# Optimization experiments

Hardware: AMD Instinct MI355X
Metric: run time of the kernel (lower is better)

The kernel has to match this reference:

```python
import jax, jax.numpy as jnp
import numpy as np

N, E, D = 100000, 1000000, 128  # nodes, edges, feature dim (in=hidden=out)
BN_EPS = 1e-5


def setup_inputs() -> dict:
    key = jax.random.key(0)
    ks = jax.random.split(key, 6)
    inp = {
        "x": jax.random.normal(ks[0], (N, D), dtype=jnp.float32),
        "edge_src": jax.random.randint(ks[1], (E,), 0, N),
        "edge_dst": jax.random.randint(ks[2], (E,), 0, N),
    }
    # GraphConv weights (xavier-ish) and biases for 3 layers
    for i in range(3):
        inp[f"W{i}"] = jax.random.normal(ks[3 + i], (D, D), dtype=jnp.float32) * np.float32(1.0 / np.sqrt(D))
        inp[f"b{i}"] = jnp.zeros((D,), dtype=jnp.float32)
    # BatchNorm (eval mode) params/buffers for the 2 inter-layer BNs
    for i in range(2):
        inp[f"bn_gamma{i}"] = jnp.ones((D,), dtype=jnp.float32)
        inp[f"bn_beta{i}"] = jnp.zeros((D,), dtype=jnp.float32)
        inp[f"bn_mean{i}"] = jnp.zeros((D,), dtype=jnp.float32)
        inp[f"bn_var{i}"] = jnp.ones((D,), dtype=jnp.float32)
    return inp


def _gcn_forward(x, edge_src, edge_dst, Ws, bs, bns):
    n = x.shape[0]
    ones = jnp.ones((edge_src.shape[0],), x.dtype)
    # DGL GraphConv norm='both': D_out^{-1/2} on source, D_in^{-1/2} on dest, degrees clamped to >=1
    deg_out = jnp.clip(jax.ops.segment_sum(ones, edge_src, num_segments=n), 1.0)
    deg_in = jnp.clip(jax.ops.segment_sum(ones, edge_dst, num_segments=n), 1.0)
    norm_src = deg_out ** -0.5
    norm_dst = deg_in ** -0.5
    h = x
    L = len(Ws)
    for i in range(L):
        hs = (h * norm_src[:, None]) @ Ws[i]                     # [N, D] dense transform first
        agg = jax.ops.segment_sum(hs[edge_src], edge_dst, num_segments=n)  # SpMM: gather + scatter-add
        h = agg * norm_dst[:, None] + bs[i]
        if i < L - 1:  # BN (eval) + activation between layers; dropout=0 -> no-op
            g, bta, m, v = bns[i]
            h = (h - m) * jax.lax.rsqrt(v + BN_EPS) * g + bta
            h = jax.nn.relu(h)
    return h


def reference(x, edge_src, edge_dst, W0, b0, W1, b1, W2, b2,
              bn_gamma0, bn_beta0, bn_mean0, bn_var0,
              bn_gamma1, bn_beta1, bn_mean1, bn_var1):
    Ws = (W0, W1, W2)
    bs = (b0, b1, b2)
    bns = ((bn_gamma0, bn_beta0, bn_mean0, bn_var0),
           (bn_gamma1, bn_beta1, bn_mean1, bn_var1))
    return _gcn_forward(x, edge_src, edge_dst, Ws, bs, bns)
```

## Files before the change

kernel.cpp:

```cpp
#include <hip/hip_runtime.h>
#include <hip/hip_fp16.h>
#include <math.h>

#define D 128
#define NSL 32
#define PBU 25088

typedef _Float16 half8 __attribute__((ext_vector_type(8)));
typedef float f32x4 __attribute__((ext_vector_type(4)));

__device__ inline uint pack_f16x2(float a, float b) {
  __half2 h = __floats2half2_rn(a, b);
  return *reinterpret_cast<uint*>(&h);
}
__device__ inline float2 unpack_f16x2(uint p) {
  __half2 h = *reinterpret_cast<__half2*>(&p);
  return __half22float2(h);
}
__device__ inline uint mdiv40(uint x, uint M) {
  return (uint)(((unsigned long long)x * M) >> 40);
}


__global__ __launch_bounds__(1024) void k_build1(const int* __restrict__ esrc,
                                                 const int* __restrict__ edst,
                                                 const float* __restrict__ W0,
                                                 const float* __restrict__ W1,
                                                 const float* __restrict__ W2,
                                                 const float* __restrict__ b0,
                                                 const float* __restrict__ b1,
                                                 const float* __restrict__ b2,
                                                 const float* __restrict__ g0,
                                                 const float* __restrict__ be0,
                                                 const float* __restrict__ mu0,
                                                 const float* __restrict__ vr0,
                                                 const float* __restrict__ g1,
                                                 const float* __restrict__ be1,
                                                 const float* __restrict__ mu1,
                                                 const float* __restrict__ vr1,
                                                 uint* __restrict__ pd,
                                                 uint* __restrict__ ps,
                                                 uchar* __restrict__ rank8,
                                                 ushort* __restrict__ Wt,
                                                 float* __restrict__ CA,
                                                 float* __restrict__ CB,
                                                 int E, int SB) {
  __shared__ uint h[PBU];
  const int b = blockIdx.x;
  const int t = threadIdx.x;
  if (b < 32) {
    for (int j = t; j < PBU; j += 1024) h[j] = 0u;
    __syncthreads();
    const int i0 = b * SB, i1 = min(i0 + SB, E);
    for (int i = i0 + t; i < i1; i += 1024) {
      const int d = edst[i];
      const uint sh = (uint)(d & 3) * 8u;
      const uint old = atomicAdd(&h[d >> 2], 1u << sh);
      rank8[i] = (uchar)((old >> sh) & 0xffu);
    }
    __syncthreads();
    uint* p = pd + (size_t)b * PBU;
    for (int j = t; j < PBU; j += 1024) p[j] = h[j];
  } else if (b < 64) {
    const int sl = b - 32;
    for (int j = t; j < PBU; j += 1024) h[j] = 0u;
    __syncthreads();
    const int i0 = sl * SB, i1 = min(i0 + SB, E);
    for (int i = i0 + t; i < i1; i += 1024) {
      const int s = esrc[i];
      atomicAdd(&h[s >> 2], 1u << ((uint)(s & 3) * 8u));
    }
    __syncthreads();
    uint* p = ps + (size_t)sl * PBU;
    for (int j = t; j < PBU; j += 1024) p[j] = h[j];
  } else if (b < 112) {
    const int li = (b - 64) * 1024 + t;
    const int l = li >> 14;
    const int i = li & 16383;
    const int n = i >> 7, k = i & 127;
    const float* W = (l == 0) ? W0 : ((l == 1) ? W1 : W2);
    Wt[li] = __half_as_ushort(__float2half_rn(W[k * D + n]));
  } else if (t < D) {
    const int c = t;
    float A0 = g0[c] * rsqrtf(vr0[c] + 1e-5f);
    CA[c] = A0;
    CB[c] = (b0[c] - mu0[c]) * A0 + be0[c];
    float A1 = g1[c] * rsqrtf(vr1[c] + 1e-5f);
    CA[D + c] = A1;
    CB[D + c] = (b1[c] - mu1[c]) * A1 + be1[c];
    CA[2 * D + c] = 1.f;
    CB[2 * D + c] = b2[c];
  }
}


__global__ __launch_bounds__(256) void k_build2(uint* __restrict__ pd,
                                                const uint* __restrict__ ps,
                                                int* __restrict__ totd,
                                                float* __restrict__ ns,
                                                float* __restrict__ nd,
                                                int* __restrict__ csum, int N) {
  __shared__ int sd[256];
  const int t = threadIdx.x;
  const int j = blockIdx.x * 256 + t;
  const int n0 = j * 4;
  uint r0 = 0, r1 = 0, r2 = 0, r3 = 0;
  uint s0 = 0, s1 = 0, s2 = 0, s3 = 0;
#pragma unroll
  for (int sl = 0; sl < NSL; ++sl) {
    const uint v = pd[(size_t)sl * PBU + j];
    pd[(size_t)sl * PBU + j] = r0 | (r1 << 8) | (r2 << 16) | (r3 << 24);
    r0 += v & 0xffu; r1 += (v >> 8) & 0xffu; r2 += (v >> 16) & 0xffu; r3 += (v >> 24) & 0xffu;
    const uint w = ps[(size_t)sl * PBU + j];
    s0 += w & 0xffu; s1 += (w >> 8) & 0xffu; s2 += (w >> 16) & 0xffu; s3 += (w >> 24) & 0xffu;
  }
  const uint rr[4] = {r0, r1, r2, r3};
  const uint ss[4] = {s0, s1, s2, s3};
  int tot = 0;
#pragma unroll
  for (int k = 0; k < 4; ++k) {
    if (n0 + k < N) {
      totd[n0 + k] = (int)rr[k];
      nd[n0 + k] = rsqrtf((float)max(rr[k], 1u));
      ns[n0 + k] = rsqrtf((float)max(ss[k], 1u));
      tot += (int)rr[k];
    }
  }
  sd[t] = tot; __syncthreads();
  for (int off = 128; off > 0; off >>= 1) {
    if (t < off) sd[t] += sd[t + off];
    __syncthreads();
  }
  if (t == 0) csum[blockIdx.x] = sd[0];
}


__global__ void k_scan_serial(int* __restrict__ csum, int nch,
                              int* __restrict__ rofs, int n) {
  if (blockIdx.x == 0 && threadIdx.x == 0) {
    int run = 0;
    for (int b = 0; b < nch; ++b) { int v = csum[b]; csum[b] = run; run += v; }
    rofs[n] = run;
  }
}

__global__ __launch_bounds__(256) void k_scan_final(const int* __restrict__ totd,
                                                    const int* __restrict__ csum,
                                                    int* __restrict__ rofs, int n) {
  __shared__ int sd[256];
  const int b = blockIdx.x, t = threadIdx.x;
  const int base = b * 1024 + t * 4;
  int v[4]; int s = 0;
#pragma unroll
  for (int i = 0; i < 4; ++i) { v[i] = (base + i < n) ? totd[base + i] : 0; s += v[i]; }
  sd[t] = s; __syncthreads();
  for (int off = 1; off < 256; off <<= 1) {
    int x = (t >= off) ? sd[t - off] : 0;
    __syncthreads();
    sd[t] += x;
    __syncthreads();
  }
  int o = sd[t] - s + csum[b];
#pragma unroll
  for (int i = 0; i < 4; ++i) {
    if (base + i < n) { rofs[base + i] = o; o += v[i]; }
  }
}


__global__ void k_scatter2(const int* __restrict__ esrc, const int* __restrict__ edst,
                           const uchar* __restrict__ rank8,
                           const uint* __restrict__ pd,
                           const int* __restrict__ rofs, int* __restrict__ csr,
                           int E, uint Msb) {
  const int i = blockIdx.x * 256 + threadIdx.x;
  if (i >= E) return;
  const int d = edst[i];
  const uint sl = mdiv40((uint)i, Msb);
  const uint pk = pd[(size_t)sl * PBU + (d >> 2)];
  const uint pfx = (pk >> ((uint)(d & 3) * 8u)) & 0xffu;
  csr[rofs[d] + (int)pfx + (int)rank8[i]] = esrc[i];
}


__global__ __launch_bounds__(256) void k_gemm32(const float* __restrict__ X,
                                                const ushort* __restrict__ Wt,
                                                const float* __restrict__ ns,
                                                ushort* __restrict__ out, int M) {
  const int lane = threadIdx.x & 63;
  const int wv = threadIdx.x >> 6;
  const int m0 = (blockIdx.x * 4 + wv) * 32;
  if (m0 >= M) return;
  const int lr = lane & 15;
  const int kg = (lane >> 4) * 8;

  half8 hf[2][4];
  const half8 hz = {};
#pragma unroll
  for (int mt = 0; mt < 2; ++mt) {
    const int row = m0 + mt * 16 + lr;
    if (row < M) {
      const float s = ns[row];
#pragma unroll
      for (int kt = 0; kt < 4; ++kt) {
        const float4 a = *reinterpret_cast<const float4*>(X + (size_t)row * D + kt * 32 + kg);
        const float4 b = *reinterpret_cast<const float4*>(X + (size_t)row * D + kt * 32 + kg + 4);
        half8 hv;
        hv[0] = (_Float16)(a.x * s); hv[1] = (_Float16)(a.y * s);
        hv[2] = (_Float16)(a.z * s); hv[3] = (_Float16)(a.w * s);
        hv[4] = (_Float16)(b.x * s); hv[5] = (_Float16)(b.y * s);
        hv[6] = (_Float16)(b.z * s); hv[7] = (_Float16)(b.w * s);
        hf[mt][kt] = hv;
      }
    } else {
#pragma unroll
      for (int kt = 0; kt < 4; ++kt) hf[mt][kt] = hz;
    }
  }

  f32x4 acc[8][2];
#pragma unroll
  for (int nt = 0; nt < 8; ++nt) { acc[nt][0] = (f32x4)(0.f); acc[nt][1] = (f32x4)(0.f); }

#pragma unroll
  for (int nt = 0; nt < 8; ++nt) {
    const ushort* wb = Wt + (size_t)(nt * 16 + lr) * D + kg;
#pragma unroll
    for (int kt = 0; kt < 4; ++kt) {
      half8 wf = *reinterpret_cast<const half8*>(wb + kt * 32);
      acc[nt][0] = __builtin_amdgcn_mfma_f32_16x16x32_f16(wf, hf[0][kt], acc[nt][0], 0, 0, 0);
      acc[nt][1] = __builtin_amdgcn_mfma_f32_16x16x32_f16(wf, hf[1][kt], acc[nt][1], 0, 0, 0);
    }
  }

  const int mo = lane & 15;
  const int no = (lane >> 4) * 4;
#pragma unroll
  for (int mt = 0; mt < 2; ++mt) {
    const int row = m0 + mt * 16 + mo;
    if (row < M) {
#pragma unroll
      for (int nt = 0; nt < 8; ++nt) {
        uint2 u;
        u.x = pack_f16x2(acc[nt][mt][0], acc[nt][mt][1]);
        u.y = pack_f16x2(acc[nt][mt][2], acc[nt][mt][3]);
        *reinterpret_cast<uint2*>(out + (size_t)row * D + nt * 16 + no) = u;
      }
    }
  }
}


__global__ __launch_bounds__(256) void k_gemm16(const ushort* __restrict__ A,
                                                const ushort* __restrict__ Wt,
                                                ushort* __restrict__ out, int M) {
  const int lane = threadIdx.x & 63;
  const int wv = threadIdx.x >> 6;
  const int m0 = (blockIdx.x * 4 + wv) * 32;
  if (m0 >= M) return;
  const int lr = lane & 15;
  const int kg = (lane >> 4) * 8;

  half8 hf[2][4];
  const half8 hz = {};
#pragma unroll
  for (int mt = 0; mt < 2; ++mt) {
    const int row = m0 + mt * 16 + lr;
    const bool ok = row < M;
#pragma unroll
    for (int kt = 0; kt < 4; ++kt)
      hf[mt][kt] = ok ? *reinterpret_cast<const half8*>(A + (size_t)row * D + kt * 32 + kg)
                      : hz;
  }

  f32x4 acc[8][2];
#pragma unroll
  for (int nt = 0; nt < 8; ++nt) { acc[nt][0] = (f32x4)(0.f); acc[nt][1] = (f32x4)(0.f); }

#pragma unroll
  for (int nt = 0; nt < 8; ++nt) {
    const ushort* wb = Wt + (size_t)(nt * 16 + lr) * D + kg;
#pragma unroll
    for (int kt = 0; kt < 4; ++kt) {
      half8 wf = *reinterpret_cast<const half8*>(wb + kt * 32);
      acc[nt][0] = __builtin_amdgcn_mfma_f32_16x16x32_f16(wf, hf[0][kt], acc[nt][0], 0, 0, 0);
      acc[nt][1] = __builtin_amdgcn_mfma_f32_16x16x32_f16(wf, hf[1][kt], acc[nt][1], 0, 0, 0);
    }
  }

  const int mo = lane & 15;
  const int no = (lane >> 4) * 4;
#pragma unroll
  for (int mt = 0; mt < 2; ++mt) {
    const int row = m0 + mt * 16 + mo;
    if (row < M) {
#pragma unroll
      for (int nt = 0; nt < 8; ++nt) {
        uint2 u;
        u.x = pack_f16x2(acc[nt][mt][0], acc[nt][mt][1]);
        u.y = pack_f16x2(acc[nt][mt][2], acc[nt][mt][3]);
        *reinterpret_cast<uint2*>(out + (size_t)row * D + nt * 16 + no) = u;
      }
    }
  }
}


__global__ __launch_bounds__(256) void k_spmm16(const uint* __restrict__ hs,
                                                const int* __restrict__ csr,
                                                const int* __restrict__ rofs,
                                                const float* __restrict__ nd,
                                                const float* __restrict__ ns,
                                                const float* __restrict__ CA,
                                                const float* __restrict__ CB,
                                                float* __restrict__ outf,
                                                uint* __restrict__ hnext,
                                                int N, int last) {
  const int t = threadIdx.x;
  const int lane = t & 63;
  const int c16 = lane & 15;
  const int gb = lane & ~15;
  const int d = blockIdx.x * 16 + (t >> 4);
  if (d >= N) return;
  const int beg = rofs[d], end = rofs[d + 1];

  float acc[8];
#pragma unroll
  for (int j = 0; j < 8; ++j) acc[j] = 0.f;

  for (int base = beg; base < end; base += 16) {
    const int len = min(16, end - base);
    const int idx = csr[min(base + c16, end - 1)];
#pragma unroll 1
    for (int j = 0; j < len; j += 4) {
      const int l1 = min(j + 1, len - 1), l2 = min(j + 2, len - 1), l3 = min(j + 3, len - 1);
      const int s0 = __shfl(idx, gb + j);
      const int s1 = __shfl(idx, gb + l1);
      const int s2 = __shfl(idx, gb + l2);
      const int s3 = __shfl(idx, gb + l3);
      const float w1 = (j + 1 < len) ? 1.f : 0.f;
      const float w2 = (j + 2 < len) ? 1.f : 0.f;
      const float w3 = (j + 3 < len) ? 1.f : 0.f;
      const uint4 v0 = *reinterpret_cast<const uint4*>(hs + (size_t)s0 * 64 + c16 * 4);
      const uint4 v1 = *reinterpret_cast<const uint4*>(hs + (size_t)s1 * 64 + c16 * 4);
      const uint4 v2 = *reinterpret_cast<const uint4*>(hs + (size_t)s2 * 64 + c16 * 4);
      const uint4 v3 = *reinterpret_cast<const uint4*>(hs + (size_t)s3 * 64 + c16 * 4);
#pragma unroll
      for (int q = 0; q < 4; ++q) {
        const uint u0 = (&v0.x)[q], u1 = (&v1.x)[q], u2 = (&v2.x)[q], u3 = (&v3.x)[q];
        const float2 a0 = unpack_f16x2(u0);
        const float2 a1 = unpack_f16x2(u1);
        const float2 a2 = unpack_f16x2(u2);
        const float2 a3 = unpack_f16x2(u3);
        acc[q * 2]     += a0.x;
        acc[q * 2 + 1] += a0.y;
        acc[q * 2]     = fmaf(a1.x, w1, acc[q * 2]);
        acc[q * 2 + 1] = fmaf(a1.y, w1, acc[q * 2 + 1]);
        acc[q * 2]     = fmaf(a2.x, w2, acc[q * 2]);
        acc[q * 2 + 1] = fmaf(a2.y, w2, acc[q * 2 + 1]);
        acc[q * 2]     = fmaf(a3.x, w3, acc[q * 2]);
        acc[q * 2 + 1] = fmaf(a3.y, w3, acc[q * 2 + 1]);
      }
    }
  }

  const float ndv = nd[d];
  const float4 ca0 = *reinterpret_cast<const float4*>(CA + c16 * 8);
  const float4 ca1 = *reinterpret_cast<const float4*>(CA + c16 * 8 + 4);
  const float4 cb0 = *reinterpret_cast<const float4*>(CB + c16 * 8);
  const float4 cb1 = *reinterpret_cast<const float4*>(CB + c16 * 8 + 4);
  float r[8];
  r[0] = acc[0] * ndv * ca0.x + cb0.x;
  r[1] = acc[1] * ndv * ca0.y + cb0.y;
  r[2] = acc[2] * ndv * ca0.z + cb0.z;
  r[3] = acc[3] * ndv * ca0.w + cb0.w;
  r[4] = acc[4] * ndv * ca1.x + cb1.x;
  r[5] = acc[5] * ndv * ca1.y + cb1.y;
  r[6] = acc[6] * ndv * ca1.z + cb1.z;
  r[7] = acc[7] * ndv * ca1.w + cb1.w;
  if (!last) {
    const float s = ns[d];
#pragma unroll
    for (int j = 0; j < 8; ++j) r[j] = fmaxf(r[j], 0.f) * s;
    uint4 u;
    u.x = pack_f16x2(r[0], r[1]);
    u.y = pack_f16x2(r[2], r[3]);
    u.z = pack_f16x2(r[4], r[5]);
    u.w = pack_f16x2(r[6], r[7]);
    *reinterpret_cast<uint4*>(hnext + (size_t)d * 64 + c16 * 4) = u;
  } else {
    float4 o0 = make_float4(r[0], r[1], r[2], r[3]);
    float4 o1 = make_float4(r[4], r[5], r[6], r[7]);
    *reinterpret_cast<float4*>(outf + (size_t)d * D + c16 * 8) = o0;
    *reinterpret_cast<float4*>(outf + (size_t)d * D + c16 * 8 + 4) = o1;
  }
}


extern "C" void kernel_launch(void* const* d_in, const int* in_sizes, int n_in,
                              void* d_out, int out_size, void* d_ws, size_t ws_size,
                              hipStream_t stream) {
  const float* x = (const float*)d_in[0];
  const int* esrc = (const int*)d_in[1];
  const int* edst = (const int*)d_in[2];
  const float* W0 = (const float*)d_in[3];
  const float* b0 = (const float*)d_in[4];
  const float* W1 = (const float*)d_in[5];
  const float* b1 = (const float*)d_in[6];
  const float* W2 = (const float*)d_in[7];
  const float* b2 = (const float*)d_in[8];
  const float* g0 = (const float*)d_in[9];
  const float* be0 = (const float*)d_in[10];
  const float* m0 = (const float*)d_in[11];
  const float* v0 = (const float*)d_in[12];
  const float* g1 = (const float*)d_in[13];
  const float* be1 = (const float*)d_in[14];
  const float* m1 = (const float*)d_in[15];
  const float* v1 = (const float*)d_in[16];
  const int N = in_sizes[0] / D;
  const int E = in_sizes[1];

  const int SB = (E + NSL - 1) / NSL;
  const uint Msb = (uint)(((1ULL << 40) + (unsigned long long)SB - 1) / (unsigned long long)SB);

  char* p = (char*)d_ws;
  auto carve = [&](size_t bytes) {
    char* r = p;
    p += (bytes + 255) & ~(size_t)255;
    return (void*)r;
  };
  uint* hs16 = (uint*)carve((size_t)N * 64 * 4);
  ushort* Wt = (ushort*)carve((size_t)3 * D * D * 2);
  float* CA = (float*)carve((size_t)3 * D * 4);
  float* CB = (float*)carve((size_t)3 * D * 4);
  float* ns = (float*)carve((size_t)N * 4);
  float* nd = (float*)carve((size_t)N * 4);
  uint* pd = (uint*)carve((size_t)NSL * PBU * 4);
  uint* ps = (uint*)carve((size_t)NSL * PBU * 4);
  uchar* rank8 = (uchar*)carve((size_t)E);
  int* totd = (int*)carve((size_t)N * 4);
  int* rofs = (int*)carve((size_t)(N + 1) * 4);
  const int nch = (N + 1023) / 1024;
  int* csum = (int*)carve((size_t)nch * 4);
  int* csr = (int*)carve((size_t)E * 4);
  uint* bufA = (uint*)d_out;

  k_build1<<<113, 1024, 0, stream>>>(esrc, edst, W0, W1, W2, b0, b1, b2,
                                     g0, be0, m0, v0, g1, be1, m1, v1,
                                     pd, ps, rank8, Wt, CA, CB, E, SB);
  k_build2<<<nch, 256, 0, stream>>>(pd, ps, totd, ns, nd, csum, N);
  k_scan_serial<<<1, 1, 0, stream>>>(csum, nch, rofs, N);
  k_scan_final<<<nch, 256, 0, stream>>>(totd, csum, rofs, N);
  k_scatter2<<<(E + 255) / 256, 256, 0, stream>>>(esrc, edst, rank8, pd, rofs, csr, E, Msb);

  const int gb = (N + 127) / 128;
  const int sb = (N + 15) / 16;
  k_gemm32<<<gb, 256, 0, stream>>>(x, Wt, ns, (ushort*)hs16, N);
  k_spmm16<<<sb, 256, 0, stream>>>(hs16, csr, rofs, nd, ns, CA, CB, nullptr, bufA, N, 0);
  k_gemm16<<<gb, 256, 0, stream>>>((const ushort*)bufA, Wt + 16384, (ushort*)hs16, N);
  k_spmm16<<<sb, 256, 0, stream>>>(hs16, csr, rofs, nd, ns, CA + D, CB + D, nullptr, bufA, N, 0);
  k_gemm16<<<gb, 256, 0, stream>>>((const ushort*)bufA, Wt + 32768, (ushort*)hs16, N);
  k_spmm16<<<sb, 256, 0, stream>>>(hs16, csr, rofs, nd, ns, CA + 2 * D, CB + 2 * D,
                                   (float*)d_out, nullptr, N, 1);
}
```

Baseline: 267.6 us.

## Fuse all graph-build, GEMM and SpMM stages into one cooperative persistent kernel

Replaces the eleven separate launches (histograms, prefix scans, CSR scatter, three GEMMs, three SpMMs) with a single cooperative kernel of 256 blocks of 1024 threads, separated by grid.sync barriers. The degree histogram is split into 128 slices per direction instead of 32 so every block takes part. Block-level scans become wave-level shuffle scans. The CSR scatter runs alongside the first GEMM. The goal is to remove launch gaps and inter-kernel drain/fill. The cost is several grid-wide barriers, and a fixed grid with one large block per CU that may reduce occupancy and latency hiding in the gather-heavy SpMM phases.

```diff
diff --git a/kernel.cpp b/kernel.cpp
--- a/kernel.cpp
+++ b/kernel.cpp
@@ -1,10 +1,15 @@
 #include <hip/hip_runtime.h>
 #include <hip/hip_fp16.h>
+#include <hip/hip_cooperative_groups.h>
 #include <math.h>
 
 #define D 128
-#define NSL 32
+#define NSL 128
 #define PBU 25088
+#define GRID 256
+#define BLK 1024
+
+namespace cg = cooperative_groups;
 
 typedef _Float16 half8 __attribute__((ext_vector_type(8)));
 typedef float f32x4 __attribute__((ext_vector_type(4)));
@@ -21,179 +26,67 @@
   return (uint)(((unsigned long long)x * M) >> 40);
 }
 
-
-__global__ __launch_bounds__(1024) void k_build1(const int* __restrict__ esrc,
-                                                 const int* __restrict__ edst,
-                                                 const float* __restrict__ W0,
-                                                 const float* __restrict__ W1,
-                                                 const float* __restrict__ W2,
-                                                 const float* __restrict__ b0,
-                                                 const float* __restrict__ b1,
-                                                 const float* __restrict__ b2,
-                                                 const float* __restrict__ g0,
-                                                 const float* __restrict__ be0,
-                                                 const float* __restrict__ mu0,
-                                                 const float* __restrict__ vr0,
-                                                 const float* __restrict__ g1,
-                                                 const float* __restrict__ be1,
-                                                 const float* __restrict__ mu1,
-                                                 const float* __restrict__ vr1,
-                                                 uint* __restrict__ pd,
-                                                 uint* __restrict__ ps,
-                                                 uchar* __restrict__ rank8,
-                                                 ushort* __restrict__ Wt,
-                                                 float* __restrict__ CA,
-                                                 float* __restrict__ CB,
-                                                 int E, int SB) {
-  __shared__ uint h[PBU];
-  const int b = blockIdx.x;
-  const int t = threadIdx.x;
-  if (b < 32) {
-    for (int j = t; j < PBU; j += 1024) h[j] = 0u;
-    __syncthreads();
-    const int i0 = b * SB, i1 = min(i0 + SB, E);
-    for (int i = i0 + t; i < i1; i += 1024) {
-      const int d = edst[i];
-      const uint sh = (uint)(d & 3) * 8u;
-      const uint old = atomicAdd(&h[d >> 2], 1u << sh);
-      rank8[i] = (uchar)((old >> sh) & 0xffu);
-    }
-    __syncthreads();
-    uint* p = pd + (size_t)b * PBU;
-    for (int j = t; j < PBU; j += 1024) p[j] = h[j];
-  } else if (b < 64) {
-    const int sl = b - 32;
-    for (int j = t; j < PBU; j += 1024) h[j] = 0u;
-    __syncthreads();
-    const int i0 = sl * SB, i1 = min(i0 + SB, E);
-    for (int i = i0 + t; i < i1; i += 1024) {
-      const int s = esrc[i];
-      atomicAdd(&h[s >> 2], 1u << ((uint)(s & 3) * 8u));
-    }
-    __syncthreads();
-    uint* p = ps + (size_t)sl * PBU;
-    for (int j = t; j < PBU; j += 1024) p[j] = h[j];
-  } else if (b < 112) {
-    const int li = (b - 64) * 1024 + t;
-    const int l = li >> 14;
-    const int i = li & 16383;
-    const int n = i >> 7, k = i & 127;
-    const float* W = (l == 0) ? W0 : ((l == 1) ? W1 : W2);
-    Wt[li] = __half_as_ushort(__float2half_rn(W[k * D + n]));
-  } else if (t < D) {
-    const int c = t;
-    float A0 = g0[c] * rsqrtf(vr0[c] + 1e-5f);
-    CA[c] = A0;
-    CB[c] = (b0[c] - mu0[c]) * A0 + be0[c];
-    float A1 = g1[c] * rsqrtf(vr1[c] + 1e-5f);
-    CA[D + c] = A1;
-    CB[D + c] = (b1[c] - mu1[c]) * A1 + be1[c];
-    CA[2 * D + c] = 1.f;
-    CB[2 * D + c] = b2[c];
-  }
-}
-
-
-__global__ __launch_bounds__(256) void k_build2(uint* __restrict__ pd,
-                                                const uint* __restrict__ ps,
-                                                int* __restrict__ totd,
-                                                float* __restrict__ ns,
-                                                float* __restrict__ nd,
-                                                int* __restrict__ csum, int N) {
-  __shared__ int sd[256];
-  const int t = threadIdx.x;
-  const int j = blockIdx.x * 256 + t;
-  const int n0 = j * 4;
-  uint r0 = 0, r1 = 0, r2 = 0, r3 = 0;
-  uint s0 = 0, s1 = 0, s2 = 0, s3 = 0;
-#pragma unroll
-  for (int sl = 0; sl < NSL; ++sl) {
-    const uint v = pd[(size_t)sl * PBU + j];
-    pd[(size_t)sl * PBU + j] = r0 | (r1 << 8) | (r2 << 16) | (r3 << 24);
-    r0 += v & 0xffu; r1 += (v >> 8) & 0xffu; r2 += (v >> 16) & 0xffu; r3 += (v >> 24) & 0xffu;
-    const uint w = ps[(size_t)sl * PBU + j];
-    s0 += w & 0xffu; s1 += (w >> 8) & 0xffu; s2 += (w >> 16) & 0xffu; s3 += (w >> 24) & 0xffu;
-  }
-  const uint rr[4] = {r0, r1, r2, r3};
-  const uint ss[4] = {s0, s1, s2, s3};
-  int tot = 0;
-#pragma unroll
-  for (int k = 0; k < 4; ++k) {
-    if (n0 + k < N) {
-      totd[n0 + k] = (int)rr[k];
-      nd[n0 + k] = rsqrtf((float)max(rr[k], 1u));
-      ns[n0 + k] = rsqrtf((float)max(ss[k], 1u));
-      tot += (int)rr[k];
-    }
-  }
-  sd[t] = tot; __syncthreads();
-  for (int off = 128; off > 0; off >>= 1) {
-    if (t < off) sd[t] += sd[t + off];
-    __syncthreads();
-  }
-  if (t == 0) csum[blockIdx.x] = sd[0];
-}
-
-
-__global__ void k_scan_serial(int* __restrict__ csum, int nch,
-                              int* __restrict__ rofs, int n) {
-  if (blockIdx.x == 0 && threadIdx.x == 0) {
-    int run = 0;
-    for (int b = 0; b < nch; ++b) { int v = csum[b]; csum[b] = run; run += v; }
-    rofs[n] = run;
-  }
-}
-
-__global__ __launch_bounds__(256) void k_scan_final(const int* __restrict__ totd,
-                                                    const int* __restrict__ csum,
-                                                    int* __restrict__ rofs, int n) {
-  __shared__ int sd[256];
-  const int b = blockIdx.x, t = threadIdx.x;
-  const int base = b * 1024 + t * 4;
-  int v[4]; int s = 0;
-#pragma unroll
-  for (int i = 0; i < 4; ++i) { v[i] = (base + i < n) ? totd[base + i] : 0; s += v[i]; }
-  sd[t] = s; __syncthreads();
-  for (int off = 1; off < 256; off <<= 1) {
-    int x = (t >= off) ? sd[t - off] : 0;
-    __syncthreads();
-    sd[t] += x;
-    __syncthreads();
-  }
-  int o = sd[t] - s + csum[b];
-#pragma unroll
-  for (int i = 0; i < 4; ++i) {
-    if (base + i < n) { rofs[base + i] = o; o += v[i]; }
-  }
-}
-
-
-__global__ void k_scatter2(const int* __restrict__ esrc, const int* __restrict__ edst,
-                           const uchar* __restrict__ rank8,
-                           const uint* __restrict__ pd,
-                           const int* __restrict__ rofs, int* __restrict__ csr,
-                           int E, uint Msb) {
-  const int i = blockIdx.x * 256 + threadIdx.x;
-  if (i >= E) return;
-  const int d = edst[i];
-  const uint sl = mdiv40((uint)i, Msb);
-  const uint pk = pd[(size_t)sl * PBU + (d >> 2)];
-  const uint pfx = (pk >> ((uint)(d & 3) * 8u)) & 0xffu;
-  csr[rofs[d] + (int)pfx + (int)rank8[i]] = esrc[i];
-}
-
-
-__global__ __launch_bounds__(256) void k_gemm32(const float* __restrict__ X,
-                                                const ushort* __restrict__ Wt,
-                                                const float* __restrict__ ns,
-                                                ushort* __restrict__ out, int M) {
-  const int lane = threadIdx.x & 63;
-  const int wv = threadIdx.x >> 6;
-  const int m0 = (blockIdx.x * 4 + wv) * 32;
+struct MegaArgs {
+  const float* x; const int* esrc; const int* edst;
+  const float* W0; const float* b0; const float* W1; const float* b1;
+  const float* W2; const float* b2;
+  const float* g0; const float* be0; const float* mu0; const float* vr0;
+  const float* g1; const float* be1; const float* mu1; const float* vr1;
+  uint* pd; uint* ps; uchar* rank8;
+  ushort* Wt; float* CA; float* CB;
+  float* ns; float* nd; int* totd; int* csum; int* rofs;
+  int* csr; uint* hs16; uint* bufA; float* outF;
+  int N, E, SB, nch2; uint Msb;
+};
+
+__device__ inline void gemm_wave_f16(const ushort* __restrict__ A,
+                                     const ushort* __restrict__ Wt,
+                                     ushort* __restrict__ out, int M, int w, int lane) {
+  const int m0 = w * 32;
   if (m0 >= M) return;
   const int lr = lane & 15;
   const int kg = (lane >> 4) * 8;
-
+  half8 hf[2][4];
+  const half8 hz = {};
+#pragma unroll
+  for (int mt = 0; mt < 2; ++mt) {
+    const int row = m0 + mt * 16 + lr;
+    const bool ok = row < M;
+#pragma unroll
+    for (int kt = 0; kt < 4; ++kt)
+      hf[mt][kt] = ok ? *reinterpret_cast<const half8*>(A + (size_t)row * D + kt * 32 + kg) : hz;
+  }
+  const int no = (lane >> 4) * 4;
+#pragma unroll
+  for (int nt = 0; nt < 8; ++nt) {
+    f32x4 a0 = (f32x4)(0.f), a1 = (f32x4)(0.f);
+    const ushort* wb = Wt + (size_t)(nt * 16 + lr) * D + kg;
+#pragma unroll
+    for (int kt = 0; kt < 4; ++kt) {
+      half8 wf = *reinterpret_cast<const half8*>(wb + kt * 32);
+      a0 = __builtin_amdgcn_mfma_f32_16x16x32_f16(wf, hf[0][kt], a0, 0, 0, 0);
+      a1 = __builtin_amdgcn_mfma_f32_16x16x32_f16(wf, hf[1][kt], a1, 0, 0, 0);
+    }
+    const int r0 = m0 + lr, r1 = m0 + 16 + lr;
+    if (r0 < M) {
+      uint2 u; u.x = pack_f16x2(a0[0], a0[1]); u.y = pack_f16x2(a0[2], a0[3]);
+      *reinterpret_cast<uint2*>(out + (size_t)r0 * D + nt * 16 + no) = u;
+    }
+    if (r1 < M) {
+      uint2 u; u.x = pack_f16x2(a1[0], a1[1]); u.y = pack_f16x2(a1[2], a1[3]);
+      *reinterpret_cast<uint2*>(out + (size_t)r1 * D + nt * 16 + no) = u;
+    }
+  }
+}
+
+__device__ inline void gemm_wave_f32(const float* __restrict__ X,
+                                     const ushort* __restrict__ Wt,
+                                     const float* __restrict__ ns,
+                                     ushort* __restrict__ out, int M, int w, int lane) {
+  const int m0 = w * 32;
+  if (m0 >= M) return;
+  const int lr = lane & 15;
+  const int kg = (lane >> 4) * 8;
   half8 hf[2][4];
   const half8 hz = {};
 #pragma unroll
@@ -217,209 +110,268 @@
       for (int kt = 0; kt < 4; ++kt) hf[mt][kt] = hz;
     }
   }
-
-  f32x4 acc[8][2];
-#pragma unroll
-  for (int nt = 0; nt < 8; ++nt) { acc[nt][0] = (f32x4)(0.f); acc[nt][1] = (f32x4)(0.f); }
-
+  const int no = (lane >> 4) * 4;
 #pragma unroll
   for (int nt = 0; nt < 8; ++nt) {
+    f32x4 a0 = (f32x4)(0.f), a1 = (f32x4)(0.f);
     const ushort* wb = Wt + (size_t)(nt * 16 + lr) * D + kg;
 #pragma unroll
     for (int kt = 0; kt < 4; ++kt) {
       half8 wf = *reinterpret_cast<const half8*>(wb + kt * 32);
-      acc[nt][0] = __builtin_amdgcn_mfma_f32_16x16x32_f16(wf, hf[0][kt], acc[nt][0], 0, 0, 0);
-      acc[nt][1] = __builtin_amdgcn_mfma_f32_16x16x32_f16(wf, hf[1][kt], acc[nt][1], 0, 0, 0);
-    }
-  }
-
-  const int mo = lane & 15;
-  const int no = (lane >> 4) * 4;
-#pragma unroll
-  for (int mt = 0; mt < 2; ++mt) {
-    const int row = m0 + mt * 16 + mo;
-    if (row < M) {
-#pragma unroll
-      for (int nt = 0; nt < 8; ++nt) {
-        uint2 u;
-        u.x = pack_f16x2(acc[nt][mt][0], acc[nt][mt][1]);
-        u.y = pack_f16x2(acc[nt][mt][2], acc[nt][mt][3]);
-        *reinterpret_cast<uint2*>(out + (size_t)row * D + nt * 16 + no) = u;
-      }
-    }
-  }
-}
-
-
-__global__ __launch_bounds__(256) void k_gemm16(const ushort* __restrict__ A,
-                                                const ushort* __restrict__ Wt,
-                                                ushort* __restrict__ out, int M) {
-  const int lane = threadIdx.x & 63;
-  const int wv = threadIdx.x >> 6;
-  const int m0 = (blockIdx.x * 4 + wv) * 32;
-  if (m0 >= M) return;
-  const int lr = lane & 15;
-  const int kg = (lane >> 4) * 8;
-
-  half8 hf[2][4];
-  const half8 hz = {};
-#pragma unroll
-  for (int mt = 0; mt < 2; ++mt) {
-    const int row = m0 + mt * 16 + lr;
-    const bool ok = row < M;
-#pragma unroll
-    for (int kt = 0; kt < 4; ++kt)
-      hf[mt][kt] = ok ? *reinterpret_cast<const half8*>(A + (size_t)row * D + kt * 32 + kg)
-                      : hz;
-  }
-
-  f32x4 acc[8][2];
-#pragma unroll
-  for (int nt = 0; nt < 8; ++nt) { acc[nt][0] = (f32x4)(0.f); acc[nt][1] = (f32x4)(0.f); }
-
-#pragma unroll
-  for (int nt = 0; nt < 8; ++nt) {
-    const ushort* wb = Wt + (size_t)(nt * 16 + lr) * D + kg;
-#pragma unroll
-    for (int kt = 0; kt < 4; ++kt) {
-      half8 wf = *reinterpret_cast<const half8*>(wb + kt * 32);
-      acc[nt][0] = __builtin_amdgcn_mfma_f32_16x16x32_f16(wf, hf[0][kt], acc[nt][0], 0, 0, 0);
-      acc[nt][1] = __builtin_amdgcn_mfma_f32_16x16x32_f16(wf, hf[1][kt], acc[nt][1], 0, 0, 0);
-    }
-  }
-
-  const int mo = lane & 15;
-  const int no = (lane >> 4) * 4;
-#pragma unroll
-  for (int mt = 0; mt < 2; ++mt) {
-    const int row = m0 + mt * 16 + mo;
-    if (row < M) {
-#pragma unroll
-      for (int nt = 0; nt < 8; ++nt) {
-        uint2 u;
-        u.x = pack_f16x2(acc[nt][mt][0], acc[nt][mt][1]);
-        u.y = pack_f16x2(acc[nt][mt][2], acc[nt][mt][3]);
-        *reinterpret_cast<uint2*>(out + (size_t)row * D + nt * 16 + no) = u;
-      }
-    }
-  }
-}
-
-
-__global__ __launch_bounds__(256) void k_spmm16(const uint* __restrict__ hs,
-                                                const int* __restrict__ csr,
-                                                const int* __restrict__ rofs,
-                                                const float* __restrict__ nd,
-                                                const float* __restrict__ ns,
-                                                const float* __restrict__ CA,
-                                                const float* __restrict__ CB,
-                                                float* __restrict__ outf,
-                                                uint* __restrict__ hnext,
-                                                int N, int last) {
-  const int t = threadIdx.x;
-  const int lane = t & 63;
+      a0 = __builtin_amdgcn_mfma_f32_16x16x32_f16(wf, hf[0][kt], a0, 0, 0, 0);
+      a1 = __builtin_amdgcn_mfma_f32_16x16x32_f16(wf, hf[1][kt], a1, 0, 0, 0);
+    }
+    const int r0 = m0 + lr, r1 = m0 + 16 + lr;
+    if (r0 < M) {
+      uint2 u; u.x = pack_f16x2(a0[0], a0[1]); u.y = pack_f16x2(a0[2], a0[3]);
+      *reinterpret_cast<uint2*>(out + (size_t)r0 * D + nt * 16 + no) = u;
+    }
+    if (r1 < M) {
+      uint2 u; u.x = pack_f16x2(a1[0], a1[1]); u.y = pack_f16x2(a1[2], a1[3]);
+      *reinterpret_cast<uint2*>(out + (size_t)r1 * D + nt * 16 + no) = u;
+    }
+  }
+}
+
+__device__ inline void spmm_phase(const uint* __restrict__ hs,
+                                  const int* __restrict__ csr,
+                                  const int* __restrict__ rofs,
+                                  const float* __restrict__ nd,
+                                  const float* __restrict__ ns,
+                                  const float* __restrict__ CA,
+                                  const float* __restrict__ CB,
+                                  float* __restrict__ outf,
+                                  uint* __restrict__ hnext,
+                                  int N, int gid, int lane, int last) {
   const int c16 = lane & 15;
   const int gb = lane & ~15;
-  const int d = blockIdx.x * 16 + (t >> 4);
-  if (d >= N) return;
-  const int beg = rofs[d], end = rofs[d + 1];
-
-  float acc[8];
-#pragma unroll
-  for (int j = 0; j < 8; ++j) acc[j] = 0.f;
-
-  for (int base = beg; base < end; base += 16) {
-    const int len = min(16, end - base);
-    const int idx = csr[min(base + c16, end - 1)];
+  for (int d = gid >> 4; d < N; d += (GRID * BLK) >> 4) {
+    const int beg = rofs[d], end = rofs[d + 1];
+    float acc[8];
+#pragma unroll
+    for (int j = 0; j < 8; ++j) acc[j] = 0.f;
+    for (int base = beg; base < end; base += 16) {
+      const int len = min(16, end - base);
+      const int idx = csr[min(base + c16, end - 1)];
 #pragma unroll 1
-    for (int j = 0; j < len; j += 4) {
-      const int l1 = min(j + 1, len - 1), l2 = min(j + 2, len - 1), l3 = min(j + 3, len - 1);
-      const int s0 = __shfl(idx, gb + j);
-      const int s1 = __shfl(idx, gb + l1);
-      const int s2 = __shfl(idx, gb + l2);
-      const int s3 = __shfl(idx, gb + l3);
-      const float w1 = (j + 1 < len) ? 1.f : 0.f;
-      const float w2 = (j + 2 < len) ? 1.f : 0.f;
-      const float w3 = (j + 3 < len) ? 1.f : 0.f;
-      const uint4 v0 = *reinterpret_cast<const uint4*>(hs + (size_t)s0 * 64 + c16 * 4);
-      const uint4 v1 = *reinterpret_cast<const uint4*>(hs + (size_t)s1 * 64 + c16 * 4);
-      const uint4 v2 = *reinterpret_cast<const uint4*>(hs + (size_t)s2 * 64 + c16 * 4);
-      const uint4 v3 = *reinterpret_cast<const uint4*>(hs + (size_t)s3 * 64 + c16 * 4);
-#pragma unroll
-      for (int q = 0; q < 4; ++q) {
-        const uint u0 = (&v0.x)[q], u1 = (&v1.x)[q], u2 = (&v2.x)[q], u3 = (&v3.x)[q];
-        const float2 a0 = unpack_f16x2(u0);
-        const float2 a1 = unpack_f16x2(u1);
-        const float2 a2 = unpack_f16x2(u2);
-        const float2 a3 = unpack_f16x2(u3);
-        acc[q * 2]     += a0.x;
-        acc[q * 2 + 1] += a0.y;
-        acc[q * 2]     = fmaf(a1.x, w1, acc[q * 2]);
-        acc[q * 2 + 1] = fmaf(a1.y, w1, acc[q * 2 + 1]);
-        acc[q * 2]     = fmaf(a2.x, w2, acc[q * 2]);
-        acc[q * 2 + 1] = fmaf(a2.y, w2, acc[q * 2 + 1]);
-        acc[q * 2]     = fmaf(a3.x, w3, acc[q * 2]);
-        acc[q * 2 + 1] = fmaf(a3.y, w3, acc[q * 2 + 1]);
-      }
-    }
-  }
-
-  const float ndv = nd[d];
-  const float4 ca0 = *reinterpret_cast<const float4*>(CA + c16 * 8);
-  const float4 ca1 = *reinterpret_cast<const float4*>(CA + c16 * 8 + 4);
-  const float4 cb0 = *reinterpret_cast<const float4*>(CB + c16 * 8);
-  const float4 cb1 = *reinterpret_cast<const float4*>(CB + c16 * 8 + 4);
-  float r[8];
-  r[0] = acc[0] * ndv * ca0.x + cb0.x;
-  r[1] = acc[1] * ndv * ca0.y + cb0.y;
-  r[2] = acc[2] * ndv * ca0.z + cb0.z;
-  r[3] = acc[3] * ndv * ca0.w + cb0.w;
-  r[4] = acc[4] * ndv * ca1.x + cb1.x;
-  r[5] = acc[5] * ndv * ca1.y + cb1.y;
-  r[6] = acc[6] * ndv * ca1.z + cb1.z;
-  r[7] = acc[7] * ndv * ca1.w + cb1.w;
-  if (!last) {
-    const float s = ns[d];
-#pragma unroll
-    for (int j = 0; j < 8; ++j) r[j] = fmaxf(r[j], 0.f) * s;
-    uint4 u;
-    u.x = pack_f16x2(r[0], r[1]);
-    u.y = pack_f16x2(r[2], r[3]);
-    u.z = pack_f16x2(r[4], r[5]);
-    u.w = pack_f16x2(r[6], r[7]);
-    *reinterpret_cast<uint4*>(hnext + (size_t)d * 64 + c16 * 4) = u;
-  } else {
-    float4 o0 = make_float4(r[0], r[1], r[2], r[3]);
-    float4 o1 = make_float4(r[4], r[5], r[6], r[7]);
-    *reinterpret_cast<float4*>(outf + (size_t)d * D + c16 * 8) = o0;
-    *reinterpret_cast<float4*>(outf + (size_t)d * D + c16 * 8 + 4) = o1;
-  }
+      for (int j = 0; j < len; j += 4) {
+        const int l1 = min(j + 1, len - 1), l2 = min(j + 2, len - 1), l3 = min(j + 3, len - 1);
+        const int s0 = __shfl(idx, gb + j);
+        const int s1 = __shfl(idx, gb + l1);
+        const int s2 = __shfl(idx, gb + l2);
+        const int s3 = __shfl(idx, gb + l3);
+        const float w1 = (j + 1 < len) ? 1.f : 0.f;
+        const float w2 = (j + 2 < len) ? 1.f : 0.f;
+        const float w3 = (j + 3 < len) ? 1.f : 0.f;
+        const uint4 v0 = *reinterpret_cast<const uint4*>(hs + (size_t)s0 * 64 + c16 * 4);
+        const uint4 v1 = *reinterpret_cast<const uint4*>(hs + (size_t)s1 * 64 + c16 * 4);
+        const uint4 v2 = *reinterpret_cast<const uint4*>(hs + (size_t)s2 * 64 + c16 * 4);
+        const uint4 v3 = *reinterpret_cast<const uint4*>(hs + (size_t)s3 * 64 + c16 * 4);
+#pragma unroll
+        for (int q = 0; q < 4; ++q) {
+          const float2 a0 = unpack_f16x2((&v0.x)[q]);
+          const float2 a1 = unpack_f16x2((&v1.x)[q]);
+          const float2 a2 = unpack_f16x2((&v2.x)[q]);
+          const float2 a3 = unpack_f16x2((&v3.x)[q]);
+          acc[q * 2]     += a0.x;
+          acc[q * 2 + 1] += a0.y;
+          acc[q * 2]     = fmaf(a1.x, w1, acc[q * 2]);
+          acc[q * 2 + 1] = fmaf(a1.y, w1, acc[q * 2 + 1]);
+          acc[q * 2]     = fmaf(a2.x, w2, acc[q * 2]);
+          acc[q * 2 + 1] = fmaf(a2.y, w2, acc[q * 2 + 1]);
+          acc[q * 2]     = fmaf(a3.x, w3, acc[q * 2]);
+          acc[q * 2 + 1] = fmaf(a3.y, w3, acc[q * 2 + 1]);
+        }
+      }
+    }
+    const float ndv = nd[d];
+    const float4 ca0 = *reinterpret_cast<const float4*>(CA + c16 * 8);
+    const float4 ca1 = *reinterpret_cast<const float4*>(CA + c16 * 8 + 4);
+    const float4 cb0 = *reinterpret_cast<const float4*>(CB + c16 * 8);
+    const float4 cb1 = *reinterpret_cast<const float4*>(CB + c16 * 8 + 4);
+    float r[8];
+    r[0] = acc[0] * ndv * ca0.x + cb0.x;
+    r[1] = acc[1] * ndv * ca0.y + cb0.y;
+    r[2] = acc[2] * ndv * ca0.z + cb0.z;
+    r[3] = acc[3] * ndv * ca0.w + cb0.w;
+    r[4] = acc[4] * ndv * ca1.x + cb1.x;
+    r[5] = acc[5] * ndv * ca1.y + cb1.y;
+    r[6] = acc[6] * ndv * ca1.z + cb1.z;
+    r[7] = acc[7] * ndv * ca1.w + cb1.w;
+    if (!last) {
+      const float s = ns[d];
+#pragma unroll
+      for (int j = 0; j < 8; ++j) r[j] = fmaxf(r[j], 0.f) * s;
+      uint4 u;
+      u.x = pack_f16x2(r[0], r[1]);
+      u.y = pack_f16x2(r[2], r[3]);
+      u.z = pack_f16x2(r[4], r[5]);
+      u.w = pack_f16x2(r[6], r[7]);
+      *reinterpret_cast<uint4*>(hnext + (size_t)d * 64 + c16 * 4) = u;
+    } else {
+      float4 o0 = make_float4(r[0], r[1], r[2], r[3]);
+      float4 o1 = make_float4(r[4], r[5], r[6], r[7]);
+      *reinterpret_cast<float4*>(outf + (size_t)d * D + c16 * 8) = o0;
+      *reinterpret_cast<float4*>(outf + (size_t)d * D + c16 * 8 + 4) = o1;
+    }
+  }
+}
+
+
+__global__ __launch_bounds__(BLK) void k_mega(MegaArgs a) {
+  __shared__ uint h[PBU];
+  cg::grid_group grid = cg::this_grid();
+  const int t = threadIdx.x;
+  const int bid = blockIdx.x;
+  const int gid = bid * BLK + t;
+  const int lane = t & 63;
+  const int wid = gid >> 6;
+
+  for (int j = t; j < PBU; j += BLK) h[j] = 0u;
+  __syncthreads();
+  {
+    const int sl = (bid < NSL) ? bid : bid - NSL;
+    const int i0 = sl * a.SB, i1 = min(i0 + a.SB, a.E);
+    if (bid < NSL) {
+      for (int i = i0 + t; i < i1; i += BLK) {
+        const int d = a.edst[i];
+        const uint sh = (uint)(d & 3) * 8u;
+        const uint old = atomicAdd(&h[d >> 2], 1u << sh);
+        a.rank8[i] = (uchar)((old >> sh) & 0xffu);
+      }
+    } else {
+      for (int i = i0 + t; i < i1; i += BLK) {
+        const int s = a.esrc[i];
+        atomicAdd(&h[s >> 2], 1u << ((uint)(s & 3) * 8u));
+      }
+    }
+  }
+  __syncthreads();
+  {
+    uint* p = ((bid < NSL) ? a.pd : a.ps) + (size_t)((bid < NSL) ? bid : bid - NSL) * PBU;
+    for (int j = t; j < PBU; j += BLK) p[j] = h[j];
+  }
+  if (gid < 3 * D * D) {
+    const int li = gid;
+    const int l = li >> 14;
+    const int i = li & 16383;
+    const int n = i >> 7, k = i & 127;
+    const float* W = (l == 0) ? a.W0 : ((l == 1) ? a.W1 : a.W2);
+    a.Wt[li] = __half_as_ushort(__float2half_rn(W[k * D + n]));
+  } else if (gid < 3 * D * D + D) {
+    const int c = gid - 3 * D * D;
+    float A0 = a.g0[c] * rsqrtf(a.vr0[c] + 1e-5f);
+    a.CA[c] = A0;
+    a.CB[c] = (a.b0[c] - a.mu0[c]) * A0 + a.be0[c];
+    float A1 = a.g1[c] * rsqrtf(a.vr1[c] + 1e-5f);
+    a.CA[D + c] = A1;
+    a.CB[D + c] = (a.b1[c] - a.mu1[c]) * A1 + a.be1[c];
+    a.CA[2 * D + c] = 1.f;
+    a.CB[2 * D + c] = a.b2[c];
+  }
+  grid.sync();
+
+  if (wid < a.nch2) {
+    const int j = wid * 64 + lane;
+    uint r0 = 0, r1 = 0, r2 = 0, r3 = 0, s0 = 0, s1 = 0, s2 = 0, s3 = 0;
+#pragma unroll 8
+    for (int sl = 0; sl < NSL; ++sl) {
+      uint* pp = a.pd + (size_t)sl * PBU + j;
+      const uint v = *pp;
+      *pp = r0 | (r1 << 8) | (r2 << 16) | (r3 << 24);
+      r0 += v & 0xffu; r1 += (v >> 8) & 0xffu; r2 += (v >> 16) & 0xffu; r3 += (v >> 24) & 0xffu;
+      const uint w = a.ps[(size_t)sl * PBU + j];
+      s0 += w & 0xffu; s1 += (w >> 8) & 0xffu; s2 += (w >> 16) & 0xffu; s3 += (w >> 24) & 0xffu;
+    }
+    const uint rr[4] = {r0, r1, r2, r3};
+    const uint ss[4] = {s0, s1, s2, s3};
+    const int n0 = j * 4;
+    int tot = 0;
+#pragma unroll
+    for (int k = 0; k < 4; ++k) {
+      if (n0 + k < a.N) {
+        a.totd[n0 + k] = (int)rr[k];
+        a.nd[n0 + k] = rsqrtf((float)max(rr[k], 1u));
+        a.ns[n0 + k] = rsqrtf((float)max(ss[k], 1u));
+        tot += (int)rr[k];
+      }
+    }
+#pragma unroll
+    for (int off = 32; off >= 1; off >>= 1) tot += __shfl_xor(tot, off);
+    if (lane == 0) a.csum[wid] = tot;
+  }
+  grid.sync();
+
+  if (bid == 0 && t < 64) {
+    int run = 0;
+    for (int b0 = 0; b0 < a.nch2; b0 += 64) {
+      const int idx = b0 + t;
+      int v = (idx < a.nch2) ? a.csum[idx] : 0;
+      int sc = v;
+#pragma unroll
+      for (int off = 1; off < 64; off <<= 1) {
+        int u = __shfl_up(sc, off);
+        if (t >= off) sc += u;
+      }
+      if (idx < a.nch2) a.csum[idx] = run + sc - v;
+      run += __shfl(sc, 63);
+    }
+    if (t == 0) a.rofs[a.N] = run;
+  }
+  grid.sync();
+
+  if (wid < a.nch2) {
+    const int base = wid * 256 + lane * 4;
+    int v[4]; int s = 0;
+#pragma unroll
+    for (int i = 0; i < 4; ++i) { v[i] = (base + i < a.N) ? a.totd[base + i] : 0; s += v[i]; }
+    int sc = s;
+#pragma unroll
+    for (int off = 1; off < 64; off <<= 1) {
+      int u = __shfl_up(sc, off);
+      if (lane >= off) sc += u;
+    }
+    int o = a.csum[wid] + sc - s;
+#pragma unroll
+    for (int i = 0; i < 4; ++i) {
+      if (base + i < a.N) { a.rofs[base + i] = o; o += v[i]; }
+    }
+  }
+  grid.sync();
+
+  for (int i = gid; i < a.E; i += GRID * BLK) {
+    const int d = a.edst[i];
+    const uint sl = mdiv40((uint)i, a.Msb);
+    const uint pk = a.pd[(size_t)sl * PBU + (d >> 2)];
+    const uint pfx = (pk >> ((uint)(d & 3) * 8u)) & 0xffu;
+    a.csr[a.rofs[d] + (int)pfx + (int)a.rank8[i]] = a.esrc[i];
+  }
+  gemm_wave_f32(a.x, a.Wt, a.ns, (ushort*)a.hs16, a.N, wid, lane);
+  grid.sync();
+
+  spmm_phase(a.hs16, a.csr, a.rofs, a.nd, a.ns, a.CA, a.CB, nullptr, a.bufA, a.N, gid, lane, 0);
+  grid.sync();
+
+  gemm_wave_f16((const ushort*)a.bufA, a.Wt + 16384, (ushort*)a.hs16, a.N, wid, lane);
+  grid.sync();
+
+  spmm_phase(a.hs16, a.csr, a.rofs, a.nd, a.ns, a.CA + D, a.CB + D, nullptr, a.bufA, a.N,
+             gid, lane, 0);
+  grid.sync();
+
+  gemm_wave_f16((const ushort*)a.bufA, a.Wt + 32768, (ushort*)a.hs16, a.N, wid, lane);
+  grid.sync();
+
+  spmm_phase(a.hs16, a.csr, a.rofs, a.nd, a.ns, a.CA + 2 * D, a.CB + 2 * D, a.outF, nullptr,
+             a.N, gid, lane, 1);
 }
 
 
 extern "C" void kernel_launch(void* const* d_in, const int* in_sizes, int n_in,
                               void* d_out, int out_size, void* d_ws, size_t ws_size,
                               hipStream_t stream) {
-  const float* x = (const float*)d_in[0];
-  const int* esrc = (const int*)d_in[1];
-  const int* edst = (const int*)d_in[2];
-  const float* W0 = (const float*)d_in[3];
-  const float* b0 = (const float*)d_in[4];
-  const float* W1 = (const float*)d_in[5];
-  const float* b1 = (const float*)d_in[6];
-  const float* W2 = (const float*)d_in[7];
-  const float* b2 = (const float*)d_in[8];
-  const float* g0 = (const float*)d_in[9];
-  const float* be0 = (const float*)d_in[10];
-  const float* m0 = (const float*)d_in[11];
-  const float* v0 = (const float*)d_in[12];
-  const float* g1 = (const float*)d_in[13];
-  const float* be1 = (const float*)d_in[14];
-  const float* m1 = (const float*)d_in[15];
-  const float* v1 = (const float*)d_in[16];
   const int N = in_sizes[0] / D;
   const int E = in_sizes[1];
-
   const int SB = (E + NSL - 1) / NSL;
   const uint Msb = (uint)(((1ULL << 40) + (unsigned long long)SB - 1) / (unsigned long long)SB);
 
@@ -440,26 +392,29 @@
   uchar* rank8 = (uchar*)carve((size_t)E);
   int* totd = (int*)carve((size_t)N * 4);
   int* rofs = (int*)carve((size_t)(N + 1) * 4);
-  const int nch = (N + 1023) / 1024;
-  int* csum = (int*)carve((size_t)nch * 4);
+  const int nch2 = (N + 255) / 256;
+  int* csum = (int*)carve((size_t)nch2 * 4);
   int* csr = (int*)carve((size_t)E * 4);
-  uint* bufA = (uint*)d_out;
-
-  k_build1<<<113, 1024, 0, stream>>>(esrc, edst, W0, W1, W2, b0, b1, b2,
-                                     g0, be0, m0, v0, g1, be1, m1, v1,
-                                     pd, ps, rank8, Wt, CA, CB, E, SB);
-  k_build2<<<nch, 256, 0, stream>>>(pd, ps, totd, ns, nd, csum, N);
-  k_scan_serial<<<1, 1, 0, stream>>>(csum, nch, rofs, N);
-  k_scan_final<<<nch, 256, 0, stream>>>(totd, csum, rofs, N);
-  k_scatter2<<<(E + 255) / 256, 256, 0, stream>>>(esrc, edst, rank8, pd, rofs, csr, E, Msb);
-
-  const int gb = (N + 127) / 128;
-  const int sb = (N + 15) / 16;
-  k_gemm32<<<gb, 256, 0, stream>>>(x, Wt, ns, (ushort*)hs16, N);
-  k_spmm16<<<sb, 256, 0, stream>>>(hs16, csr, rofs, nd, ns, CA, CB, nullptr, bufA, N, 0);
-  k_gemm16<<<gb, 256, 0, stream>>>((const ushort*)bufA, Wt + 16384, (ushort*)hs16, N);
-  k_spmm16<<<sb, 256, 0, stream>>>(hs16, csr, rofs, nd, ns, CA + D, CB + D, nullptr, bufA, N, 0);
-  k_gemm16<<<gb, 256, 0, stream>>>((const ushort*)bufA, Wt + 32768, (ushort*)hs16, N);
-  k_spmm16<<<sb, 256, 0, stream>>>(hs16, csr, rofs, nd, ns, CA + 2 * D, CB + 2 * D,
-                                   (float*)d_out, nullptr, N, 1);
-}
+
+  MegaArgs args;
+  args.x = (const float*)d_in[0];
+  args.esrc = (const int*)d_in[1];
+  args.edst = (const int*)d_in[2];
+  args.W0 = (const float*)d_in[3];  args.b0 = (const float*)d_in[4];
+  args.W1 = (const float*)d_in[5];  args.b1 = (const float*)d_in[6];
+  args.W2 = (const float*)d_in[7];  args.b2 = (const float*)d_in[8];
+  args.g0 = (const float*)d_in[9];  args.be0 = (const float*)d_in[10];
+  args.mu0 = (const float*)d_in[11]; args.vr0 = (const float*)d_in[12];
+  args.g1 = (const float*)d_in[13]; args.be1 = (const float*)d_in[14];
+  args.mu1 = (const float*)d_in[15]; args.vr1 = (const float*)d_in[16];
+  args.pd = pd; args.ps = ps; args.rank8 = rank8;
+  args.Wt = Wt; args.CA = CA; args.CB = CB;
+  args.ns = ns; args.nd = nd; args.totd = totd; args.csum = csum; args.rofs = rofs;
+  args.csr = csr; args.hs16 = hs16;
+  args.bufA = (uint*)d_out;
+  args.outF = (float*)d_out;
+  args.N = N; args.E = E; args.SB = SB; args.nch2 = nch2; args.Msb = Msb;
+
+  void* kp[] = {&args};
+  hipLaunchCooperativeKernel((const void*)k_mega, dim3(GRID), dim3(BLK), kp, 0, stream);
+}
```

After: 538.9 us. +101.4%, slower.

## Fuse block-sum scan into build2 via last-block ticket; merge scatter with first GEMM

Applied to the files above, without the earlier changes.

The serial single-thread scan of block sums becomes a last-block-done pattern inside k_build2, where the final block runs a wavefront shuffle scan. The CSR scatter kernel and the first dense GEMM are merged into one launch, split by block index, so the two independent workloads overlap. This removes two kernel launches and the serial scan. In exchange it adds a memset for the ticket counter and threadfence/atomic ordering requirements.

```diff
diff --git a/kernel.cpp b/kernel.cpp
--- a/kernel.cpp
+++ b/kernel.cpp
@@ -94,13 +94,17 @@
 }
 
 
-__global__ __launch_bounds__(256) void k_build2(uint* __restrict__ pd,
-                                                const uint* __restrict__ ps,
-                                                int* __restrict__ totd,
-                                                float* __restrict__ ns,
-                                                float* __restrict__ nd,
-                                                int* __restrict__ csum, int N) {
+__global__ __launch_bounds__(256) void k_build2s(uint* __restrict__ pd,
+                                                 const uint* __restrict__ ps,
+                                                 int* __restrict__ totd,
+                                                 float* __restrict__ ns,
+                                                 float* __restrict__ nd,
+                                                 int* __restrict__ csum,
+                                                 int* __restrict__ rofs,
+                                                 int* __restrict__ ticket,
+                                                 int N, int nch) {
   __shared__ int sd[256];
+  __shared__ int lastf;
   const int t = threadIdx.x;
   const int j = blockIdx.x * 256 + t;
   const int n0 = j * 4;
@@ -131,18 +135,32 @@
     if (t < off) sd[t] += sd[t + off];
     __syncthreads();
   }
-  if (t == 0) csum[blockIdx.x] = sd[0];
-}
-
-
-__global__ void k_scan_serial(int* __restrict__ csum, int nch,
-                              int* __restrict__ rofs, int n) {
-  if (blockIdx.x == 0 && threadIdx.x == 0) {
+  if (t == 0) {
+    csum[blockIdx.x] = sd[0];
+    __threadfence();
+    lastf = (atomicAdd(ticket, 1) == nch - 1) ? 1 : 0;
+  }
+  __syncthreads();
+  if (lastf && t < 64) {
+    __threadfence();
     int run = 0;
-    for (int b = 0; b < nch; ++b) { int v = csum[b]; csum[b] = run; run += v; }
-    rofs[n] = run;
-  }
-}
+    for (int b0 = 0; b0 < nch; b0 += 64) {
+      const int idx = b0 + t;
+      int v = (idx < nch) ? __hip_atomic_load(&csum[idx], __ATOMIC_RELAXED,
+                                              __HIP_MEMORY_SCOPE_AGENT) : 0;
+      int sc = v;
+#pragma unroll
+      for (int off = 1; off < 64; off <<= 1) {
+        int u = __shfl_up(sc, off);
+        if (t >= off) sc += u;
+      }
+      if (idx < nch) csum[idx] = run + sc - v;
+      run += __shfl(sc, 63);
+    }
+    if (t == 0) rofs[N] = run;
+  }
+}
+
 
 __global__ __launch_bounds__(256) void k_scan_final(const int* __restrict__ totd,
                                                     const int* __restrict__ csum,
@@ -168,25 +186,28 @@
 }
 
 
-__global__ void k_scatter2(const int* __restrict__ esrc, const int* __restrict__ edst,
-                           const uchar* __restrict__ rank8,
-                           const uint* __restrict__ pd,
-                           const int* __restrict__ rofs, int* __restrict__ csr,
-                           int E, uint Msb) {
-  const int i = blockIdx.x * 256 + threadIdx.x;
-  if (i >= E) return;
-  const int d = edst[i];
-  const uint sl = mdiv40((uint)i, Msb);
-  const uint pk = pd[(size_t)sl * PBU + (d >> 2)];
-  const uint pfx = (pk >> ((uint)(d & 3) * 8u)) & 0xffu;
-  csr[rofs[d] + (int)pfx + (int)rank8[i]] = esrc[i];
-}
-
-
-__global__ __launch_bounds__(256) void k_gemm32(const float* __restrict__ X,
-                                                const ushort* __restrict__ Wt,
-                                                const float* __restrict__ ns,
-                                                ushort* __restrict__ out, int M) {
+__global__ __launch_bounds__(256) void k_sg(const float* __restrict__ X,
+                                            const ushort* __restrict__ Wt,
+                                            const float* __restrict__ ns,
+                                            ushort* __restrict__ out,
+                                            const int* __restrict__ esrc,
+                                            const int* __restrict__ edst,
+                                            const uchar* __restrict__ rank8,
+                                            const uint* __restrict__ pd,
+                                            const int* __restrict__ rofs,
+                                            int* __restrict__ csr,
+                                            int M, int E, uint Msb, int GB) {
+  if ((int)blockIdx.x >= GB) {
+    const int i = ((int)blockIdx.x - GB) * 256 + threadIdx.x;
+    if (i < E) {
+      const int d = edst[i];
+      const uint sl = mdiv40((uint)i, Msb);
+      const uint pk = pd[(size_t)sl * PBU + (d >> 2)];
+      const uint pfx = (pk >> ((uint)(d & 3) * 8u)) & 0xffu;
+      csr[rofs[d] + (int)pfx + (int)rank8[i]] = esrc[i];
+    }
+    return;
+  }
   const int lane = threadIdx.x & 63;
   const int wv = threadIdx.x >> 6;
   const int m0 = (blockIdx.x * 4 + wv) * 32;
@@ -442,20 +463,22 @@
   int* rofs = (int*)carve((size_t)(N + 1) * 4);
   const int nch = (N + 1023) / 1024;
   int* csum = (int*)carve((size_t)nch * 4);
+  int* ticket = (int*)carve(256);
   int* csr = (int*)carve((size_t)E * 4);
   uint* bufA = (uint*)d_out;
 
+  hipMemsetAsync(ticket, 0, 4, stream);
   k_build1<<<113, 1024, 0, stream>>>(esrc, edst, W0, W1, W2, b0, b1, b2,
                                      g0, be0, m0, v0, g1, be1, m1, v1,
                                      pd, ps, rank8, Wt, CA, CB, E, SB);
-  k_build2<<<nch, 256, 0, stream>>>(pd, ps, totd, ns, nd, csum, N);
-  k_scan_serial<<<1, 1, 0, stream>>>(csum, nch, rofs, N);
+  k_build2s<<<nch, 256, 0, stream>>>(pd, ps, totd, ns, nd, csum, rofs, ticket, N, nch);
   k_scan_final<<<nch, 256, 0, stream>>>(totd, csum, rofs, N);
-  k_scatter2<<<(E + 255) / 256, 256, 0, stream>>>(esrc, edst, rank8, pd, rofs, csr, E, Msb);
 
   const int gb = (N + 127) / 128;
   const int sb = (N + 15) / 16;
-  k_gemm32<<<gb, 256, 0, stream>>>(x, Wt, ns, (ushort*)hs16, N);
+  const int scb = (E + 255) / 256;
+  k_sg<<<gb + scb, 256, 0, stream>>>(x, Wt, ns, (ushort*)hs16, esrc, edst, rank8, pd, rofs,
+                                     csr, N, E, Msb, gb);
   k_spmm16<<<sb, 256, 0, stream>>>(hs16, csr, rofs, nd, ns, CA, CB, nullptr, bufA, N, 0);
   k_gemm16<<<gb, 256, 0, stream>>>((const ushort*)bufA, Wt + 16384, (ushort*)hs16, N);
   k_spmm16<<<sb, 256, 0, stream>>>(hs16, csr, rofs, nd, ns, CA + D, CB + D, nullptr, bufA, N, 0);
```

New measurement: 251.7 us. 1.06x faster.
